# Optimization experiments

Measured on AMD Instinct MI355X. Metric: run time of the kernel, lower is better.

## Reference

```python
import jax, jax.numpy as jnp
import numpy as np

N_NODES = 12288
N_EDGES = 393216  # N_NODES * avg_degree 32
IN_DIM, H1, H2 = 1433, 32, 16


def setup_inputs() -> dict:
    key = jax.random.key(0)
    ks = jax.random.split(key, 7)

    def glorot(k, fan_in, fan_out):
        r = np.sqrt(6.0 / (fan_in + fan_out)).astype(np.float32)
        return jax.random.uniform(k, (fan_in, fan_out), jnp.float32, -r, r)

    return {
        "X": jax.random.normal(ks[0], (N_NODES, IN_DIM), jnp.float32),
        "W1": glorot(ks[1], IN_DIM, H1),
        "W2": glorot(ks[2], H1, H1),
        "W3": glorot(ks[3], H1, H2),
        "edge_val": jax.random.uniform(ks[4], (N_EDGES,), jnp.float32),
        "edge_row": jax.random.randint(ks[5], (N_EDGES,), 0, N_NODES, jnp.int32),
        "edge_col": jax.random.randint(ks[6], (N_EDGES,), 0, N_NODES, jnp.int32),
    }


def reference(X, W1, W2, W3, edge_val, edge_row, edge_col):
    n = X.shape[0]

    def spmm(x):
        # sparse adj (COO) @ x : gather source rows, scale, scatter-add to dest
        return jax.ops.segment_sum(edge_val[:, None] * x[edge_col], edge_row, num_segments=n)

    h = jax.nn.relu(spmm(X @ W1))       # [N, 32]
    h = jax.nn.relu(spmm(h @ W2))       # [N, 32]
    Z = spmm(h @ W3)                    # [N, 16] (identity activation)
    A_pred = jax.nn.sigmoid(Z @ Z.T)    # [N, N] dot-product decode
    return (A_pred, Z)
```

## Files before the change

kernel.cpp:

```cpp
#include <hip/hip_runtime.h>


constexpr int NN = 12288;
constexpr int NE = 393216;
constexpr int KD = 1433;
constexpr int CAP = 96;

typedef float f32x4 __attribute__((ext_vector_type(4)));
typedef float f32x16 __attribute__((ext_vector_type(16)));
typedef short shortx8 __attribute__((ext_vector_type(8)));

constexpr int KC = 384;
constexpr int G1B = (NN / 64) * 4;

__global__ __launch_bounds__(256) void k_scatter_gemm1(const int* __restrict__ er,
                                                       const int* __restrict__ ec,
                                                       const float* __restrict__ ev,
                                                       int* __restrict__ cnt,
                                                       uint2* __restrict__ ebuf,
                                                       const float* __restrict__ X,
                                                       const float* __restrict__ W,
                                                       float* __restrict__ out) {
    if (blockIdx.x >= G1B) {
        int e = (blockIdx.x - G1B) * 256 + threadIdx.x;
        int r = er[e];
        int p = atomicAdd(&cnt[r], 1);
        if (p < CAP) ebuf[(size_t)r * CAP + p] = make_uint2((unsigned)ec[e], __float_as_uint(ev[e]));
        return;
    }
    __shared__ float ws[KC * 32];
    int rg = blockIdx.x >> 2;
    int s  = blockIdx.x & 3;
    int k0 = s * KC;
    int kt = min(KC, KD - k0);
    int tid = threadIdx.x;
    int c4 = (tid & 7) * 4;
    int rs = tid >> 3;
    int r0 = rg * 64 + rs;
    int r1 = r0 + 32;
    const float* x0 = X + (size_t)r0 * KD;
    const float* x1 = X + (size_t)r1 * KD;
    f32x4 acc0 = {0.f, 0.f, 0.f, 0.f};
    f32x4 acc1 = {0.f, 0.f, 0.f, 0.f};
    int h = (4 - (r0 & 3)) & 3;

    int n4 = (kt * 32) >> 2;
    for (int q = tid; q < n4; q += 256)
        *(f32x4*)(ws + q * 4) = *(const f32x4*)(W + (size_t)k0 * 32 + q * 4);
    __syncthreads();

    for (int kk = 0; kk < h; ++kk) {
        float a0 = x0[k0 + kk], a1 = x1[k0 + kk];
        const float* wr = ws + kk * 32 + c4;
#pragma unroll
        for (int j = 0; j < 4; ++j) { acc0[j] += a0 * wr[j]; acc1[j] += a1 * wr[j]; }
    }
    int nv = (kt - h) >> 2;
    const f32x4* p0 = (const f32x4*)(x0 + k0 + h);
    const f32x4* p1 = (const f32x4*)(x1 + k0 + h);
#pragma unroll 8
    for (int q = 0; q < nv; ++q) {
        f32x4 a0 = p0[q], a1 = p1[q];
        int kb = h + q * 4;
#pragma unroll
        for (int m = 0; m < 4; ++m) {
            f32x4 w4 = *(const f32x4*)(ws + (kb + m) * 32 + c4);
#pragma unroll
            for (int j = 0; j < 4; ++j) { acc0[j] += a0[m] * w4[j]; acc1[j] += a1[m] * w4[j]; }
        }
    }
    for (int kk = h + nv * 4; kk < kt; ++kk) {
        float a0 = x0[k0 + kk], a1 = x1[k0 + kk];
        const float* wr = ws + kk * 32 + c4;
#pragma unroll
        for (int j = 0; j < 4; ++j) { acc0[j] += a0 * wr[j]; acc1[j] += a1 * wr[j]; }
    }
#pragma unroll
    for (int j = 0; j < 4; ++j) {
        atomicAdd(&out[(size_t)r0 * 32 + c4 + j], acc0[j]);
        atomicAdd(&out[(size_t)r1 * 32 + c4 + j], acc1[j]);
    }
}

template <int CO>
__global__ __launch_bounds__(256) void spmm_gemm(const float* __restrict__ in,
                                                 const float* __restrict__ Wm,
                                                 float* __restrict__ out,
                                                 const int* __restrict__ cnt,
                                                 const uint2* __restrict__ ebuf) {
    int tid = blockIdx.x * 256 + threadIdx.x;
    int r = tid >> 6;
    int lane = threadIdx.x & 63;
    int c = lane & 31, half = lane >> 5;
    int co = c & (CO - 1);
    float wcol[32];
#pragma unroll
    for (int k = 0; k < 32; ++k) wcol[k] = Wm[k * CO + co];
    int deg = min(cnt[r], CAP);
    int mid = (deg >> 1) & ~1;
    int lo = half ? mid : 0;
    int hi = half ? deg : mid;
    const uint2* eb2 = ebuf + (size_t)r * CAP;
    const uint4* eb4 = (const uint4*)eb2;
    float acc = 0.f;
    int i = lo;
#pragma unroll 2
    for (; i + 4 <= hi; i += 4) {
        uint4 e01 = eb4[i >> 1], e23 = eb4[(i >> 1) + 1];
        acc += __uint_as_float(e01.y) * in[(size_t)e01.x * 32 + c];
        acc += __uint_as_float(e01.w) * in[(size_t)e01.z * 32 + c];
        acc += __uint_as_float(e23.y) * in[(size_t)e23.x * 32 + c];
        acc += __uint_as_float(e23.w) * in[(size_t)e23.z * 32 + c];
    }
    for (; i < hi; ++i) {
        uint2 e = eb2[i];
        acc += __uint_as_float(e.y) * in[(size_t)e.x * 32 + c];
    }
    float h = fmaxf(acc + __shfl_xor(acc, 32), 0.f);
    float o = 0.f;
#pragma unroll
    for (int k = 0; k < 32; ++k)
        o += __shfl(h, (lane & 32) + k) * wcol[k];
    if (half == 0 && c < CO) out[(size_t)r * CO + co] = o;
}

__global__ __launch_bounds__(256) void spmm16(const float* __restrict__ in,
                                              float* __restrict__ out,
                                              unsigned short* __restrict__ zb,
                                              const int* __restrict__ cnt,
                                              const uint2* __restrict__ ebuf) {
    int tid = blockIdx.x * 256 + threadIdx.x;
    int r = tid >> 5;
    int sub = tid & 31;
    int c = sub & 15, half = sub >> 4;
    int deg = min(cnt[r], CAP);
    int mid = (deg >> 1) & ~1;
    int lo = half ? mid : 0;
    int hi = half ? deg : mid;
    const uint2* eb2 = ebuf + (size_t)r * CAP;
    const uint4* eb4 = (const uint4*)eb2;
    float acc = 0.f;
    int i = lo;
#pragma unroll 2
    for (; i + 4 <= hi; i += 4) {
        uint4 e01 = eb4[i >> 1], e23 = eb4[(i >> 1) + 1];
        acc += __uint_as_float(e01.y) * in[(size_t)e01.x * 16 + c];
        acc += __uint_as_float(e01.w) * in[(size_t)e01.z * 16 + c];
        acc += __uint_as_float(e23.y) * in[(size_t)e23.x * 16 + c];
        acc += __uint_as_float(e23.w) * in[(size_t)e23.z * 16 + c];
    }
    for (; i < hi; ++i) {
        uint2 e = eb2[i];
        acc += __uint_as_float(e.y) * in[(size_t)e.x * 16 + c];
    }
    float sv = acc + __shfl_xor(acc, 16);
    if (half == 0) {
        out[(size_t)r * 16 + c] = sv;
        unsigned int bits = __float_as_uint(sv);
        zb[(size_t)r * 16 + c] = (unsigned short)((bits + 0x7FFFu + ((bits >> 16) & 1u)) >> 16);
    }
}

__global__ __launch_bounds__(256) void decode_mfma(const unsigned short* __restrict__ Zb,
                                                   float* __restrict__ A) {
    int id = blockIdx.x;
    int f = (id & 7) * (9216 / 8) + (id >> 3);
    int bi = f / 48, bj = f % 48;
    int w = threadIdx.x >> 6;
    int l = threadIdx.x & 63;
    int R = bi * 64;
    int C = bj * 256 + w * 64;
    int lr = l & 31, lh = l >> 5;

    shortx8 a0 = *(const shortx8*)(Zb + ((size_t)(R + lr) << 4) + lh * 8);
    shortx8 a1 = *(const shortx8*)(Zb + ((size_t)(R + 32 + lr) << 4) + lh * 8);
    shortx8 b0 = *(const shortx8*)(Zb + ((size_t)(C + lr) << 4) + lh * 8);
    shortx8 b1 = *(const shortx8*)(Zb + ((size_t)(C + 32 + lr) << 4) + lh * 8);

    f32x16 acc00 = {0.f}, acc01 = {0.f}, acc10 = {0.f}, acc11 = {0.f};
    acc00 = __builtin_amdgcn_mfma_f32_32x32x16_bf16(a0, b0, acc00, 0, 0, 0);
    acc01 = __builtin_amdgcn_mfma_f32_32x32x16_bf16(a0, b1, acc01, 0, 0, 0);
    acc10 = __builtin_amdgcn_mfma_f32_32x32x16_bf16(a1, b0, acc10, 0, 0, 0);
    acc11 = __builtin_amdgcn_mfma_f32_32x32x16_bf16(a1, b1, acc11, 0, 0, 0);

#pragma unroll
    for (int q = 0; q < 16; ++q) {
        int rf = (q & 3) + 8 * (q >> 2) + 4 * lh;
        float s00 = __fdividef(1.0f, 1.0f + __expf(-acc00[q]));
        float s01 = __fdividef(1.0f, 1.0f + __expf(-acc01[q]));
        float s10 = __fdividef(1.0f, 1.0f + __expf(-acc10[q]));
        float s11 = __fdividef(1.0f, 1.0f + __expf(-acc11[q]));
        __builtin_nontemporal_store(s00, &A[(size_t)(R + rf) * NN + C + lr]);
        __builtin_nontemporal_store(s01, &A[(size_t)(R + rf) * NN + C + 32 + lr]);
        __builtin_nontemporal_store(s10, &A[(size_t)(R + 32 + rf) * NN + C + lr]);
        __builtin_nontemporal_store(s11, &A[(size_t)(R + 32 + rf) * NN + C + 32 + lr]);
    }
}

extern "C" void kernel_launch(void* const* d_in, const int* in_sizes, int n_in,
                              void* d_out, int out_size, void* d_ws, size_t ws_size,
                              hipStream_t stream) {
    const float* X  = (const float*)d_in[0];
    const float* W1 = (const float*)d_in[1];
    const float* W2 = (const float*)d_in[2];
    const float* W3 = (const float*)d_in[3];
    const float* ev = (const float*)d_in[4];
    const int*   er = (const int*)d_in[5];
    const int*   ec = (const int*)d_in[6];

    float* A = (float*)d_out;
    float* Z = A + (size_t)NN * NN;

    int*   cnt = (int*)d_ws;
    float* t1 = (float*)(cnt + NN);
    float* t2 = t1 + (size_t)NN * 32;
    float* t3 = t2 + (size_t)NN * 32;
    unsigned short* Zb = (unsigned short*)t1;

    uint2* ebuf = (uint2*)(A + (size_t)140000000);

    (void)hipMemsetAsync(cnt, 0, NN * sizeof(int) + (size_t)NN * 32 * sizeof(float), stream);

    k_scatter_gemm1<<<G1B + NE / 256, 256, 0, stream>>>(er, ec, ev, cnt, ebuf, X, W1, t1);

    spmm_gemm<32><<<NN * 64 / 256, 256, 0, stream>>>(t1, W2, t2, cnt, ebuf);
    spmm_gemm<16><<<NN * 64 / 256, 256, 0, stream>>>(t2, W3, t3, cnt, ebuf);
    spmm16<<<NN * 32 / 256, 256, 0, stream>>>(t3, Z, Zb, cnt, ebuf);

    decode_mfma<<<192 * 48, 256, 0, stream>>>(Zb, A);
}
```

Baseline: 218.9 us.

## Compute first-layer GEMM with bf16 MFMA from shared-memory tiles

The X@W1 part of the fused scatter/GEMM kernel now stages a 64-row X tile and a transposed W1 chunk in shared memory as bf16, then accumulates with 32x32x16 bf16 MFMA instructions instead of scalar fp32 FMAs. The K dimension is split into six 256-wide chunks instead of four 384-wide ones, which creates more blocks. Partial sums are still combined with atomicAdd. Rounding X and W1 to bf16 lowers precision of the first layer, and the kernel is likely bound by reading X from memory anyway.

```diff
diff --git a/kernel.cpp b/kernel.cpp
--- a/kernel.cpp
+++ b/kernel.cpp
@@ -10,8 +10,15 @@
 typedef float f32x16 __attribute__((ext_vector_type(16)));
 typedef short shortx8 __attribute__((ext_vector_type(8)));
 
-constexpr int KC = 384;
-constexpr int G1B = (NN / 64) * 4;
+__device__ __forceinline__ unsigned short f2bf(float v) {
+    unsigned int b = __float_as_uint(v);
+    return (unsigned short)((b + 0x7FFFu + ((b >> 16) & 1u)) >> 16);
+}
+
+constexpr int KC = 256;
+constexpr int NCH = 6;
+constexpr int XST = KC + 8;
+constexpr int G1B = (NN / 64) * NCH;
 
 __global__ __launch_bounds__(256) void k_scatter_gemm1(const int* __restrict__ er,
                                                        const int* __restrict__ ec,
@@ -28,57 +35,63 @@
         if (p < CAP) ebuf[(size_t)r * CAP + p] = make_uint2((unsigned)ec[e], __float_as_uint(ev[e]));
         return;
     }
-    __shared__ float ws[KC * 32];
-    int rg = blockIdx.x >> 2;
-    int s  = blockIdx.x & 3;
-    int k0 = s * KC;
+    __shared__ unsigned short xs[64 * XST];
+    __shared__ unsigned short wt[32 * XST];
+
+    int rgB   = blockIdx.x / NCH;
+    int chunk = blockIdx.x % NCH;
+    int r0 = rgB * 64;
+    int k0 = chunk * KC;
     int kt = min(KC, KD - k0);
-    int tid = threadIdx.x;
-    int c4 = (tid & 7) * 4;
-    int rs = tid >> 3;
-    int r0 = rg * 64 + rs;
-    int r1 = r0 + 32;
-    const float* x0 = X + (size_t)r0 * KD;
-    const float* x1 = X + (size_t)r1 * KD;
-    f32x4 acc0 = {0.f, 0.f, 0.f, 0.f};
-    f32x4 acc1 = {0.f, 0.f, 0.f, 0.f};
-    int h = (4 - (r0 & 3)) & 3;
-
-    int n4 = (kt * 32) >> 2;
-    for (int q = tid; q < n4; q += 256)
-        *(f32x4*)(ws + q * 4) = *(const f32x4*)(W + (size_t)k0 * 32 + q * 4);
+    int nm = (kt + 15) >> 4;
+    int t = threadIdx.x;
+
+    int wtot = nm * 16 * 32;
+    for (int e = t; e < wtot; e += 256) {
+        int k = e >> 5, c = e & 31;
+        float v = (k < kt) ? W[(size_t)(k0 + k) * 32 + c] : 0.f;
+        wt[c * XST + k] = f2bf(v);
+    }
+    {
+        int r = t & 63, s = t >> 6;
+        int row = r0 + r;
+        const float* xr = X + (size_t)row * KD + k0;
+        unsigned short* xrow = xs + r * XST;
+        int h = (4 - (row & 3)) & 3;
+        if (s == 0)
+            for (int kk = 0; kk < h; ++kk) xrow[kk] = f2bf(xr[kk]);
+        int nq = (kt - h) >> 2;
+        const f32x4* xq = (const f32x4*)(xr + h);
+        for (int q = s; q < nq; q += 4) {
+            f32x4 v = xq[q];
+            int kb = h + q * 4;
+            xrow[kb + 0] = f2bf(v[0]);
+            xrow[kb + 1] = f2bf(v[1]);
+            xrow[kb + 2] = f2bf(v[2]);
+            xrow[kb + 3] = f2bf(v[3]);
+        }
+        if (s == 1)
+            for (int kk = h + nq * 4; kk < kt; ++kk) xrow[kk] = f2bf(xr[kk]);
+        if (s == 2)
+            for (int kk = kt; kk < nm * 16; ++kk) xrow[kk] = 0;
+    }
     __syncthreads();
 
-    for (int kk = 0; kk < h; ++kk) {
-        float a0 = x0[k0 + kk], a1 = x1[k0 + kk];
-        const float* wr = ws + kk * 32 + c4;
-#pragma unroll
-        for (int j = 0; j < 4; ++j) { acc0[j] += a0 * wr[j]; acc1[j] += a1 * wr[j]; }
-    }
-    int nv = (kt - h) >> 2;
-    const f32x4* p0 = (const f32x4*)(x0 + k0 + h);
-    const f32x4* p1 = (const f32x4*)(x1 + k0 + h);
-#pragma unroll 8
-    for (int q = 0; q < nv; ++q) {
-        f32x4 a0 = p0[q], a1 = p1[q];
-        int kb = h + q * 4;
-#pragma unroll
-        for (int m = 0; m < 4; ++m) {
-            f32x4 w4 = *(const f32x4*)(ws + (kb + m) * 32 + c4);
-#pragma unroll
-            for (int j = 0; j < 4; ++j) { acc0[j] += a0[m] * w4[j]; acc1[j] += a1[m] * w4[j]; }
-        }
-    }
-    for (int kk = h + nv * 4; kk < kt; ++kk) {
-        float a0 = x0[k0 + kk], a1 = x1[k0 + kk];
-        const float* wr = ws + kk * 32 + c4;
-#pragma unroll
-        for (int j = 0; j < 4; ++j) { acc0[j] += a0 * wr[j]; acc1[j] += a1 * wr[j]; }
-    }
-#pragma unroll
-    for (int j = 0; j < 4; ++j) {
-        atomicAdd(&out[(size_t)r0 * 32 + c4 + j], acc0[j]);
-        atomicAdd(&out[(size_t)r1 * 32 + c4 + j], acc1[j]);
+    int w = t >> 6, l = t & 63;
+    int rg = w >> 1;
+    int lr = l & 31, lh = l >> 5;
+    const unsigned short* xbase = xs + (rg * 32 + lr) * XST + lh * 8;
+    const unsigned short* wbase = wt + lr * XST + lh * 8;
+    f32x16 acc = {0.f};
+    for (int m = (w & 1); m < nm; m += 2) {
+        shortx8 a = *(const shortx8*)(xbase + m * 16);
+        shortx8 b = *(const shortx8*)(wbase + m * 16);
+        acc = __builtin_amdgcn_mfma_f32_32x32x16_bf16(a, b, acc, 0, 0, 0);
+    }
+#pragma unroll
+    for (int q = 0; q < 16; ++q) {
+        int rf = (q & 3) + 8 * (q >> 2) + 4 * lh;
+        atomicAdd(&out[(size_t)(r0 + rg * 32 + rf) * 32 + lr], acc[q]);
     }
 }
 
@@ -156,8 +169,7 @@
     float sv = acc + __shfl_xor(acc, 16);
     if (half == 0) {
         out[(size_t)r * 16 + c] = sv;
-        unsigned int bits = __float_as_uint(sv);
-        zb[(size_t)r * 16 + c] = (unsigned short)((bits + 0x7FFFu + ((bits >> 16) & 1u)) >> 16);
+        zb[(size_t)r * 16 + c] = f2bf(sv);
     }
 }
 
```

After: 213.4 us. 1.03x faster.
